# Kernel optimization log

Hardware: AMD Instinct MI355X
Metric: run time of the kernel (lower is better)

Reference implementation:

```python
import jax, jax.numpy as jnp
import numpy as np
import math

H = 8          # num_heads
DH = 16        # dim_head
DEPTH = 1
LAMBDA_INIT = 0.8 - 0.6 * math.exp(-0.3 * DEPTH)
LN_EPS = 1e-5


def setup_inputs() -> dict:
    key = jax.random.key(0)
    ks = jax.random.split(key, 12)
    dim = 256
    inner = 2 * H * DH  # 256
    b, n = 2, 2048
    s = lambda fan_in: 1.0 / math.sqrt(fan_in)
    return {
        "x": jax.random.normal(ks[0], (b, n, dim), jnp.float32),
        "Wq": jax.random.normal(ks[1], (dim, inner), jnp.float32) * s(dim),
        "Wkv": jax.random.normal(ks[2], (dim, 2 * inner), jnp.float32) * s(dim),
        "Wout": jax.random.normal(ks[3], (inner, dim), jnp.float32) * s(inner),
        "bout": jnp.zeros((dim,), jnp.float32),
        "Wg": jax.random.normal(ks[4], (dim, inner), jnp.float32) * s(dim),
        "bg": jnp.ones((inner,), jnp.float32),
        "lq1": jax.random.normal(ks[5], (DH,), jnp.float32) * 0.1,
        "lk1": jax.random.normal(ks[6], (DH,), jnp.float32) * 0.1,
        "lq2": jax.random.normal(ks[7], (DH,), jnp.float32) * 0.1,
        "lk2": jax.random.normal(ks[8], (DH,), jnp.float32) * 0.1,
        "ln_gamma": jnp.ones((2 * DH,), jnp.float32),
        "ln_beta": jnp.zeros((2 * DH,), jnp.float32),
    }


def reference(x, Wq, Wkv, Wout, bout, Wg, bg, lq1, lk1, lq2, lk2, ln_gamma, ln_beta):
    b, n, dim = x.shape
    scale = DH ** (-0.5)

    q = x @ Wq                                   # [b, n, 2*H*DH]
    kv = x @ Wkv                                 # [b, n, 4*H*DH]
    k, v = jnp.split(kv, 2, axis=-1)

    # doubled heads for q, k; normal heads with width 2*DH for v
    q = q.reshape(b, n, 2 * H, DH).transpose(0, 2, 1, 3) * scale  # [b, 2H, n, DH]
    k = k.reshape(b, n, 2 * H, DH).transpose(0, 2, 1, 3)          # [b, 2H, n, DH]
    v = v.reshape(b, n, H, 2 * DH).transpose(0, 2, 1, 3)          # [b, H, n, 2DH]

    dots = jnp.einsum('bhid,bhjd->bhij', q, k)   # [b, 2H, n, n]
    attn = jax.nn.softmax(dots, axis=-1)

    lam1 = jnp.exp(jnp.sum(lq1 * lk1))
    lam2 = jnp.exp(jnp.sum(lq2 * lk2))
    lam = lam1 - lam2 + LAMBDA_INIT

    attn = attn.reshape(b, H, 2, n, n)
    attn = attn[:, :, 0] - lam * attn[:, :, 1]   # [b, H, n, n]

    out = jnp.einsum('bhij,bhjd->bhid', attn, v)  # [b, H, n, 2DH]

    # LayerNorm over last dim (2*DH)
    mu = jnp.mean(out, axis=-1, keepdims=True)
    var = jnp.var(out, axis=-1, keepdims=True)
    out = (out - mu) * jax.lax.rsqrt(var + LN_EPS) * ln_gamma + ln_beta

    out = out * (1.0 - LAMBDA_INIT)
    out = out.transpose(0, 2, 1, 3).reshape(b, n, H * 2 * DH)  # [b, n, inner]

    gates = x @ Wg + bg
    out = out * jax.nn.sigmoid(gates)
    return out @ Wout + bout
```

## Files before the change

kernel.cpp:

```cpp
#include <hip/hip_runtime.h>
#include <hip/hip_bf16.h>

#define LAMBDA_INIT_F 0.35550906759096927f
#define ONE_MINUS_LI  0.64449093240903073f
#define QSCALE 0.36067376022224085f

typedef unsigned short u16;
typedef unsigned int   u32;
typedef short s4v  __attribute__((ext_vector_type(4)));
typedef float f16v __attribute__((ext_vector_type(16)));

__device__ __forceinline__ u16 f2bf(float f) {
    __hip_bfloat16 h = __float2bfloat16(f);
    return *reinterpret_cast<u16*>(&h);
}
__device__ __forceinline__ u32 pk2bf(float lo, float hi) {
    return (u32)f2bf(lo) | ((u32)f2bf(hi) << 16);
}
union U2S { u32 u[2]; s4v s; };
__device__ __forceinline__ s4v mks4(u32 a, u32 b) { U2S x; x.u[0]=a; x.u[1]=b; return x.s; }

__device__ __forceinline__ float fexp2(float x) {
#if __has_builtin(__builtin_amdgcn_exp2f)
    return __builtin_amdgcn_exp2f(x);
#else
    float r; asm volatile("v_exp_f32 %0, %1\n\ts_nop 1" : "=v"(r) : "v"(x)); return r;
#endif
}

#define MFMA(a,b,c) __builtin_amdgcn_mfma_f32_32x32x8bf16_1k((a),(b),(c),0,0,0)

__global__ __launch_bounds__(256) void prep_kernel(
    const float* __restrict__ Wq, const float* __restrict__ Wkv,
    const float* __restrict__ Wg, const float* __restrict__ Wout,
    const float* __restrict__ x,
    u16* __restrict__ WT, u16* __restrict__ xbf)
{
    const int bid = blockIdx.x;
    const int tid = threadIdx.x;

    if (bid >= 80) {
        const int r0 = (bid - 80) * 64;
        const float2* src = (const float2*)(x + (size_t)r0 * 256);
        u32* dst = (u32*)(xbf + (size_t)r0 * 256);
        for (int idx = tid; idx < 64 * 128; idx += 256) {
            float2 v = src[idx];
            dst[idx] = pk2bf(v.x, v.y);
        }
        return;
    }

    __shared__ u16 tile[16 * 258];
    const int n0g = bid * 16;
    const float* src; int cols; int ncol0;
    if      (n0g < 256)  { src = Wq;   cols = 256; ncol0 = n0g; }
    else if (n0g < 768)  { src = Wkv;  cols = 512; ncol0 = n0g - 256; }
    else if (n0g < 1024) { src = Wg;   cols = 256; ncol0 = n0g - 768; }
    else                 { src = Wout; cols = 256; ncol0 = n0g - 1024; }

    const float* srow = src + (size_t)tid * cols + ncol0;
#pragma unroll
    for (int j = 0; j < 8; ++j) {
        const float2 v = *(const float2*)(srow + 2*j);
        tile[(2*j + 0) * 258 + tid] = f2bf(v.x);
        tile[(2*j + 1) * 258 + tid] = f2bf(v.y);
    }
    __syncthreads();

    const u32* t32 = (const u32*)tile;
    const int nn = tid >> 4, part = tid & 15;
    u32* dst = (u32*)WT + (size_t)(n0g + nn) * 128 + part * 8;
    const u32* s2 = t32 + nn * 129 + part * 8;
#pragma unroll
    for (int j = 0; j < 8; ++j) dst[j] = s2[j];
}

__global__ __launch_bounds__(256) void proj_kernel(
    const u16* __restrict__ x, const u16* __restrict__ WT,
    const float* __restrict__ bg,
    u16* __restrict__ Qb, u16* __restrict__ Kb,
    u16* __restrict__ Vb, float* __restrict__ Gb)
{
    const int bid = blockIdx.x;
    const int nt = bid & 15, mt = bid >> 4;
    const int tid = threadIdx.x, w = tid >> 6, lane = tid & 63;
    const int l31 = lane & 31, hh = lane >> 5;
    const int m0 = mt * 128 + w * 32;
    const int n0 = nt * 64;

    const u16* xr  = x  + (size_t)(m0 + l31) * 256 + 4*hh;
    const u16* br0 = WT + (size_t)(n0 + l31) * 256 + 4*hh;
    const u16* br1 = WT + (size_t)(n0 + 32 + l31) * 256 + 4*hh;

    f16v a0, a1;
#pragma unroll
    for (int r = 0; r < 16; ++r) { a0[r] = 0.f; a1[r] = 0.f; }

#pragma unroll
    for (int ks = 0; ks < 16; ++ks) {
        s4v xa  = *(const s4v*)(xr  + ks*16);
        s4v xb  = *(const s4v*)(xr  + ks*16 + 8);
        s4v w0a = *(const s4v*)(br0 + ks*16);
        s4v w0b = *(const s4v*)(br0 + ks*16 + 8);
        s4v w1a = *(const s4v*)(br1 + ks*16);
        s4v w1b = *(const s4v*)(br1 + ks*16 + 8);
        a0 = MFMA(xa, w0a, a0); a0 = MFMA(xb, w0b, a0);
        a1 = MFMA(xa, w1a, a1); a1 = MFMA(xb, w1b, a1);
    }

    const int cat = nt >> 2;
#pragma unroll
    for (int ns = 0; ns < 2; ++ns) {
        const f16v& acc = ns ? a1 : a0;
        const int n = nt * 64 + ns * 32 + l31;
#pragma unroll
        for (int r = 0; r < 16; ++r) {
            const int il = (r & 3) + 8*(r >> 2) + 4*hh;
            const int R = m0 + il;
            const int b = R >> 11, i = R & 2047;
            const float v = acc[r];
            if (cat == 0) {
                const int h = n >> 4, d = n & 15;
                Qb[((size_t)(b*16 + h) * 2048 + i) * 16 + d] = f2bf(v * QSCALE);
            } else if (cat == 1) {
                const int nk = n - 256, h = nk >> 4, d = nk & 15;
                Kb[((size_t)(b*16 + h) * 2048 + i) * 16 + d] = f2bf(v);
            } else if (cat == 2) {
                const int nv = n - 512, hv = nv >> 5, d2 = nv & 31;
                Vb[((size_t)(b*8 + hv) * 2048 + i) * 32 + d2] = f2bf(v);
            } else {
                const int gcol = n - 768;
                const float t = v + bg[gcol];
                Gb[(size_t)R * 256 + gcol] = 1.0f / (1.0f + __expf(-t));
            }
        }
    }
}

__global__ __launch_bounds__(256) void attn_kernel(
    const u16* __restrict__ Q, const u16* __restrict__ K,
    const u16* __restrict__ V, const float* __restrict__ G,
    const float* __restrict__ lq1, const float* __restrict__ lk1,
    const float* __restrict__ lq2, const float* __restrict__ lk2,
    const float* __restrict__ gamma, const float* __restrict__ beta,
    u16* __restrict__ A)
{
    __shared__ float smemf[4480];
    u16* st  = (u16*)smemf;
    u32* stu = (u32*)smemf;

    const int bid = blockIdx.x;
    const int itile = bid & 63;
    const int combo = bid >> 6;
    const int ho = combo & 7, b = combo >> 3;
    const int i0 = itile * 32;

    const int tid = threadIdx.x, w = tid >> 6, lane = tid & 63;
    const int l31 = lane & 31, hh = lane >> 5;
    const int s = w & 1, jh = w >> 1;

    const u16* Kg = K + (size_t)(b*16 + 2*ho + s) * 2048 * 16;
    const u16* Vg = V + (size_t)(b*8 + ho) * 2048 * 32;
    const u16* Qg = Q + ((size_t)(b*16 + 2*ho + s) * 2048 + (i0 + l31)) * 16;
    const s4v qf0 = *(const s4v*)(Qg + 4*hh);
    const s4v qf1 = *(const s4v*)(Qg + 8 + 4*hh);

    const int jr = lane >> 1, half = lane & 1;
    const u32* kgp = (const u32*)Kg + (size_t)(jh*1024 + jr) * 8 + half*4;
    const u32* vgp = (const u32*)Vg + (size_t)(jh*1024 + jr) * 16 + s*8 + half*4;

    const int kw_off = w*288 + jr*9 + half*4;
    const int vw_u16 = 2304 + jh*1088;
    const int vd0 = s*16 + half*8;

    f16v oacc;
#pragma unroll
    for (int r = 0; r < 16; ++r) oacc[r] = 0.f;
    float lacc = 0.f;

    {
        u32 k0 = kgp[0], k1 = kgp[1], k2 = kgp[2], k3 = kgp[3];
        u32 v0 = vgp[0], v1 = vgp[1], v2 = vgp[2], v3 = vgp[3];
        u32* kd = stu + kw_off;
        kd[0]=k0; kd[1]=k1; kd[2]=k2; kd[3]=k3;
        u16* vd = st + vw_u16;
        vd[(vd0+0)*34 + jr] = (u16)(v0 & 0xffff); vd[(vd0+1)*34 + jr] = (u16)(v0 >> 16);
        vd[(vd0+2)*34 + jr] = (u16)(v1 & 0xffff); vd[(vd0+3)*34 + jr] = (u16)(v1 >> 16);
        vd[(vd0+4)*34 + jr] = (u16)(v2 & 0xffff); vd[(vd0+5)*34 + jr] = (u16)(v2 >> 16);
        vd[(vd0+6)*34 + jr] = (u16)(v3 & 0xffff); vd[(vd0+7)*34 + jr] = (u16)(v3 >> 16);
    }

    for (int c = 0; c < 32; ++c) {
        __syncthreads();
        const int p = c & 1, pn = 1 - p;

        u32 nk0=0,nk1=0,nk2=0,nk3=0, nv0=0,nv1=0,nv2=0,nv3=0;
        if (c + 1 < 32) {
            const u32* kp = kgp + (size_t)(c+1)*256;
            nk0=kp[0]; nk1=kp[1]; nk2=kp[2]; nk3=kp[3];
            const u32* vp = vgp + (size_t)(c+1)*512;
            nv0=vp[0]; nv1=vp[1]; nv2=vp[2]; nv3=vp[3];
        }

        const u32* kb2 = stu + p*2240 + w*288;
        const u32* vb2 = stu + p*2240 + 1152 + jh*544;

        f16v sc;
#pragma unroll
        for (int r = 0; r < 16; ++r) sc[r] = 0.f;
        {
            const int kidx = l31*9 + 2*hh;
            s4v kf0 = mks4(kb2[kidx],     kb2[kidx + 1]);
            sc = MFMA(kf0, qf0, sc);
            s4v kf1 = mks4(kb2[kidx + 4], kb2[kidx + 5]);
            sc = MFMA(kf1, qf1, sc);
        }
        float pv[16];
#pragma unroll
        for (int r = 0; r < 16; ++r) { pv[r] = fexp2(sc[r]); lacc += pv[r]; }
#pragma unroll
        for (int f = 0; f < 4; ++f) {
            u32 plo = __builtin_amdgcn_perm(__float_as_uint(pv[4*f+1]),
                                            __float_as_uint(pv[4*f+0]), 0x07060302);
            u32 phi = __builtin_amdgcn_perm(__float_as_uint(pv[4*f+3]),
                                            __float_as_uint(pv[4*f+2]), 0x07060302);
            s4v pf = mks4(plo, phi);
            const int vidx = l31*17 + 4*f + 2*hh;
            s4v vf = mks4(vb2[vidx], vb2[vidx + 1]);
            oacc = MFMA(pf, vf, oacc);
        }

        if (c + 1 < 32) {
            u32* kd = stu + pn*2240 + kw_off;
            kd[0]=nk0; kd[1]=nk1; kd[2]=nk2; kd[3]=nk3;
            u16* vd = st + pn*4480 + vw_u16;
            vd[(vd0+0)*34 + jr] = (u16)(nv0 & 0xffff); vd[(vd0+1)*34 + jr] = (u16)(nv0 >> 16);
            vd[(vd0+2)*34 + jr] = (u16)(nv1 & 0xffff); vd[(vd0+3)*34 + jr] = (u16)(nv1 >> 16);
            vd[(vd0+4)*34 + jr] = (u16)(nv2 & 0xffff); vd[(vd0+5)*34 + jr] = (u16)(nv2 >> 16);
            vd[(vd0+6)*34 + jr] = (u16)(nv3 & 0xffff); vd[(vd0+7)*34 + jr] = (u16)(nv3 >> 16);
        }
    }

    __syncthreads();
    float ltot = lacc + __shfl_xor(lacc, 32);
    float* ob = smemf + w * 1056;
#pragma unroll
    for (int r = 0; r < 16; ++r) {
        const int il = (r & 3) + 8*(r >> 2) + 4*hh;
        ob[il*33 + l31] = oacc[r];
    }
    if (lane < 32) smemf[4224 + w*32 + l31] = ltot;
    __syncthreads();

    if (tid < 32) {
        const int ii = tid;
        const float l1 = smemf[4224 + ii]      + smemf[4224 + 64 + ii];
        const float l2 = smemf[4224 + 32 + ii] + smemf[4224 + 96 + ii];

        float sA = 0.f, sB = 0.f;
#pragma unroll
        for (int d = 0; d < 16; ++d) {
            sA += lq1[d] * lk1[d];
            sB += lq2[d] * lk2[d];
        }
        const float lam = __expf(sA) - __expf(sB) + LAMBDA_INIT_F;
        const float c1 = 1.f / l1, c2 = lam / l2;

        float od[32], mu = 0.f;
#pragma unroll
        for (int d = 0; d < 32; ++d) {
            const float o1 = smemf[ii*33 + d]        + smemf[2112 + ii*33 + d];
            const float o2 = smemf[1056 + ii*33 + d] + smemf[3168 + ii*33 + d];
            od[d] = o1 * c1 - o2 * c2;
            mu += od[d];
        }
        mu *= (1.f / 32.f);
        float var = 0.f;
#pragma unroll
        for (int d = 0; d < 32; ++d) { const float t2 = od[d] - mu; var += t2 * t2; }
        var *= (1.f / 32.f);
        const float rs = rsqrtf(var + 1e-5f);

        const int R = b*2048 + i0 + ii;
        const float* Gr = G + (size_t)R * 256 + ho*32;
        u16* Ar = A + (size_t)R * 256 + ho*32;
#pragma unroll
        for (int d = 0; d < 32; ++d) {
            const float val = (od[d] - mu)*rs*gamma[d] + beta[d];
            Ar[d] = f2bf(val * ONE_MINUS_LI * Gr[d]);
        }
    }
}

__global__ __launch_bounds__(512) void out_kernel(
    const u16* __restrict__ Abf, const u16* __restrict__ WT,
    const float* __restrict__ bout, float* __restrict__ out)
{
    __shared__ float cs[4][32 * 33];

    const int bid = blockIdx.x;
    const int nt = bid & 3, mt = bid >> 2;
    const int tid = threadIdx.x, w = tid >> 6, lane = tid & 63;
    const int l31 = lane & 31, hh = lane >> 5;
    const int t = w >> 1, kh = w & 1;
    const int m0 = mt * 64 + (t & 1) * 32;
    const int n0 = nt * 64 + (t >> 1) * 32;

    const u16* ar = Abf + (size_t)(m0 + l31) * 256 + kh*128 + 4*hh;
    const u16* br = WT + (size_t)(1024 + n0 + l31) * 256 + kh*128 + 4*hh;

    f16v acc;
#pragma unroll
    for (int r = 0; r < 16; ++r) acc[r] = 0.f;

#pragma unroll
    for (int ks = 0; ks < 8; ++ks) {
        s4v aa = *(const s4v*)(ar + ks*16);
        s4v ab = *(const s4v*)(ar + ks*16 + 8);
        s4v ba = *(const s4v*)(br + ks*16);
        s4v bb = *(const s4v*)(br + ks*16 + 8);
        acc = MFMA(aa, ba, acc);
        acc = MFMA(ab, bb, acc);
    }

    if (kh == 0) {
#pragma unroll
        for (int r = 0; r < 16; ++r) {
            const int il = (r & 3) + 8*(r >> 2) + 4*hh;
            cs[t][il*33 + l31] = acc[r];
        }
    }
    __syncthreads();
    if (kh == 1) {
        const float bv = bout[n0 + l31];
#pragma unroll
        for (int r = 0; r < 16; ++r) {
            const int il = (r & 3) + 8*(r >> 2) + 4*hh;
            const int m = m0 + il;
            out[(size_t)m * 256 + n0 + l31] = acc[r] + cs[t][il*33 + l31] + bv;
        }
    }
}

extern "C" void kernel_launch(void* const* d_in, const int* in_sizes, int n_in,
                              void* d_out, int out_size, void* d_ws, size_t ws_size,
                              hipStream_t stream) {
    const float* x    = (const float*)d_in[0];
    const float* Wq   = (const float*)d_in[1];
    const float* Wkv  = (const float*)d_in[2];
    const float* Wout = (const float*)d_in[3];
    const float* bout = (const float*)d_in[4];
    const float* Wg   = (const float*)d_in[5];
    const float* bg   = (const float*)d_in[6];
    const float* lq1  = (const float*)d_in[7];
    const float* lk1  = (const float*)d_in[8];
    const float* lq2  = (const float*)d_in[9];
    const float* lk2  = (const float*)d_in[10];
    const float* lng  = (const float*)d_in[11];
    const float* lnb  = (const float*)d_in[12];

    u16*   WT  = (u16*)d_ws;
    u16*   xbf = WT + 327680;
    u16*   Qb  = xbf + 1048576;
    u16*   Kb  = Qb + 1048576;
    u16*   Vb  = Kb + 1048576;
    float* Gb  = (float*)(Vb + 1048576);
    u16*   Abf = (u16*)(Gb + 1048576);

    hipLaunchKernelGGL(prep_kernel, dim3(144), dim3(256), 0, stream,
                       Wq, Wkv, Wg, Wout, x, WT, xbf);
    hipLaunchKernelGGL(proj_kernel, dim3(512), dim3(256), 0, stream,
                       xbf, WT, bg, Qb, Kb, Vb, Gb);
    hipLaunchKernelGGL(attn_kernel, dim3(1024), dim3(256), 0, stream,
                       Qb, Kb, Vb, Gb, lq1, lk1, lq2, lk2, lng, lnb, Abf);
    hipLaunchKernelGGL(out_kernel, dim3(256), dim3(512), 0, stream,
                       Abf, WT, bout, (float*)d_out);
}
```

Baseline: 167.3 us.

## Give each wave a private K/V LDS staging region and drop block barriers

Every wave now stages its own copy of the K and V tiles in a separate double-buffered LDS region. Each lane loads a full 32-wide V row half instead of splitting it across the two sub-heads. This removes the per-iteration __syncthreads in the 32-step key loop, since a wave only reads data it wrote itself. The cost is duplicated V global loads across waves and a larger shared memory footprint (about 26 KB instead of 18 KB), which may reduce occupancy.

```diff
diff --git a/kernel.cpp b/kernel.cpp
--- a/kernel.cpp
+++ b/kernel.cpp
@@ -145,7 +145,7 @@
     const float* __restrict__ gamma, const float* __restrict__ beta,
     u16* __restrict__ A)
 {
-    __shared__ float smemf[4480];
+    __shared__ float smemf[6656];
     u16* st  = (u16*)smemf;
     u32* stu = (u32*)smemf;
 
@@ -166,12 +166,16 @@
     const s4v qf1 = *(const s4v*)(Qg + 8 + 4*hh);
 
     const int jr = lane >> 1, half = lane & 1;
+    const int vjr = lane >> 1, vhalf = lane & 1;
     const u32* kgp = (const u32*)Kg + (size_t)(jh*1024 + jr) * 8 + half*4;
-    const u32* vgp = (const u32*)Vg + (size_t)(jh*1024 + jr) * 16 + s*8 + half*4;
-
-    const int kw_off = w*288 + jr*9 + half*4;
-    const int vw_u16 = 2304 + jh*1088;
-    const int vd0 = s*16 + half*8;
+    const u32* vgp = (const u32*)Vg + (size_t)(jh*1024 + vjr) * 16 + vhalf*8;
+
+    const int wbase   = w * 1664;
+    const int kw_off  = wbase + jr*9 + half*4;
+    const int kr_off  = wbase + l31*9 + 2*hh;
+    const int vw_u16  = wbase*2 + 576 + vjr;
+    const int vr_off  = wbase + 288 + l31*17;
+    const int d0w     = vhalf * 16;
 
     f16v oacc;
 #pragma unroll
@@ -180,39 +184,44 @@
 
     {
         u32 k0 = kgp[0], k1 = kgp[1], k2 = kgp[2], k3 = kgp[3];
-        u32 v0 = vgp[0], v1 = vgp[1], v2 = vgp[2], v3 = vgp[3];
+        u32 nv[8];
+#pragma unroll
+        for (int q = 0; q < 8; ++q) nv[q] = vgp[q];
         u32* kd = stu + kw_off;
         kd[0]=k0; kd[1]=k1; kd[2]=k2; kd[3]=k3;
         u16* vd = st + vw_u16;
-        vd[(vd0+0)*34 + jr] = (u16)(v0 & 0xffff); vd[(vd0+1)*34 + jr] = (u16)(v0 >> 16);
-        vd[(vd0+2)*34 + jr] = (u16)(v1 & 0xffff); vd[(vd0+3)*34 + jr] = (u16)(v1 >> 16);
-        vd[(vd0+4)*34 + jr] = (u16)(v2 & 0xffff); vd[(vd0+5)*34 + jr] = (u16)(v2 >> 16);
-        vd[(vd0+6)*34 + jr] = (u16)(v3 & 0xffff); vd[(vd0+7)*34 + jr] = (u16)(v3 >> 16);
+#pragma unroll
+        for (int q = 0; q < 8; ++q) {
+            const int d = d0w + 2*q;
+            vd[(d+0)*34] = (u16)(nv[q] & 0xffff);
+            vd[(d+1)*34] = (u16)(nv[q] >> 16);
+        }
     }
 
     for (int c = 0; c < 32; ++c) {
-        __syncthreads();
         const int p = c & 1, pn = 1 - p;
 
-        u32 nk0=0,nk1=0,nk2=0,nk3=0, nv0=0,nv1=0,nv2=0,nv3=0;
+        u32 nk0=0,nk1=0,nk2=0,nk3=0, nv[8];
+#pragma unroll
+        for (int q = 0; q < 8; ++q) nv[q] = 0;
         if (c + 1 < 32) {
             const u32* kp = kgp + (size_t)(c+1)*256;
             nk0=kp[0]; nk1=kp[1]; nk2=kp[2]; nk3=kp[3];
             const u32* vp = vgp + (size_t)(c+1)*512;
-            nv0=vp[0]; nv1=vp[1]; nv2=vp[2]; nv3=vp[3];
-        }
-
-        const u32* kb2 = stu + p*2240 + w*288;
-        const u32* vb2 = stu + p*2240 + 1152 + jh*544;
+#pragma unroll
+            for (int q = 0; q < 8; ++q) nv[q] = vp[q];
+        }
+
+        const u32* kb2 = stu + p*832 + kr_off;
+        const u32* vb2 = stu + p*832 + vr_off;
 
         f16v sc;
 #pragma unroll
         for (int r = 0; r < 16; ++r) sc[r] = 0.f;
         {
-            const int kidx = l31*9 + 2*hh;
-            s4v kf0 = mks4(kb2[kidx],     kb2[kidx + 1]);
+            s4v kf0 = mks4(kb2[0], kb2[1]);
             sc = MFMA(kf0, qf0, sc);
-            s4v kf1 = mks4(kb2[kidx + 4], kb2[kidx + 5]);
+            s4v kf1 = mks4(kb2[4], kb2[5]);
             sc = MFMA(kf1, qf1, sc);
         }
         float pv[16];
@@ -225,19 +234,20 @@
             u32 phi = __builtin_amdgcn_perm(__float_as_uint(pv[4*f+3]),
                                             __float_as_uint(pv[4*f+2]), 0x07060302);
             s4v pf = mks4(plo, phi);
-            const int vidx = l31*17 + 4*f + 2*hh;
-            s4v vf = mks4(vb2[vidx], vb2[vidx + 1]);
+            s4v vf = mks4(vb2[4*f + 2*hh], vb2[4*f + 2*hh + 1]);
             oacc = MFMA(pf, vf, oacc);
         }
 
         if (c + 1 < 32) {
-            u32* kd = stu + pn*2240 + kw_off;
+            u32* kd = stu + pn*832 + kw_off;
             kd[0]=nk0; kd[1]=nk1; kd[2]=nk2; kd[3]=nk3;
-            u16* vd = st + pn*4480 + vw_u16;
-            vd[(vd0+0)*34 + jr] = (u16)(nv0 & 0xffff); vd[(vd0+1)*34 + jr] = (u16)(nv0 >> 16);
-            vd[(vd0+2)*34 + jr] = (u16)(nv1 & 0xffff); vd[(vd0+3)*34 + jr] = (u16)(nv1 >> 16);
-            vd[(vd0+4)*34 + jr] = (u16)(nv2 & 0xffff); vd[(vd0+5)*34 + jr] = (u16)(nv2 >> 16);
-            vd[(vd0+6)*34 + jr] = (u16)(nv3 & 0xffff); vd[(vd0+7)*34 + jr] = (u16)(nv3 >> 16);
+            u16* vd = st + pn*1664 + vw_u16;
+#pragma unroll
+            for (int q = 0; q < 8; ++q) {
+                const int d = d0w + 2*q;
+                vd[(d+0)*34] = (u16)(nv[q] & 0xffff);
+                vd[(d+1)*34] = (u16)(nv[q] >> 16);
+            }
         }
     }
 
```

Result: no change. 166.1 us (-0.7%).

## Split attention work across query tiles instead of key halves to share K/V tiles

Applied to the files above, without the earlier changes.

The attention kernel now gives each block 64 query rows, split across warp pairs, instead of 32 query rows with the key range split between warp pairs. Every warp now walks all 64 key chunks, and the staged K/V tiles in shared memory are shared by both query sub-tiles, which halves global K/V traffic per query row and halves the grid. The row-sum accumulator is also split into two independent chains to shorten dependency latency. In exchange each warp runs twice as many serial loop iterations with more barriers, grid occupancy drops to 512 blocks, and the final combine stage uses 64 threads.

```diff
diff --git a/kernel.cpp b/kernel.cpp
--- a/kernel.cpp
+++ b/kernel.cpp
@@ -150,74 +150,76 @@
     u32* stu = (u32*)smemf;
 
     const int bid = blockIdx.x;
-    const int itile = bid & 63;
-    const int combo = bid >> 6;
+    const int itile = bid & 31;
+    const int combo = bid >> 5;
     const int ho = combo & 7, b = combo >> 3;
-    const int i0 = itile * 32;
+    const int i0 = itile * 64;
 
     const int tid = threadIdx.x, w = tid >> 6, lane = tid & 63;
     const int l31 = lane & 31, hh = lane >> 5;
-    const int s = w & 1, jh = w >> 1;
-
-    const u16* Kg = K + (size_t)(b*16 + 2*ho + s) * 2048 * 16;
+    const int s = w & 1, it = w >> 1;
+    const int i0w = i0 + it * 32;
+
     const u16* Vg = V + (size_t)(b*8 + ho) * 2048 * 32;
-    const u16* Qg = Q + ((size_t)(b*16 + 2*ho + s) * 2048 + (i0 + l31)) * 16;
+    const u16* Qg = Q + ((size_t)(b*16 + 2*ho + s) * 2048 + (i0w + l31)) * 16;
     const s4v qf0 = *(const s4v*)(Qg + 4*hh);
     const s4v qf1 = *(const s4v*)(Qg + 8 + 4*hh);
 
-    const int jr = lane >> 1, half = lane & 1;
-    const u32* kgp = (const u32*)Kg + (size_t)(jh*1024 + jr) * 8 + half*4;
-    const u32* vgp = (const u32*)Vg + (size_t)(jh*1024 + jr) * 16 + s*8 + half*4;
-
-    const int kw_off = w*288 + jr*9 + half*4;
-    const int vw_u16 = 2304 + jh*1088;
-    const int vd0 = s*16 + half*8;
+    const int ksub = tid >> 7, krow = (tid >> 2) & 31, kseg = tid & 3;
+    const u32* kgp = (const u32*)(K + (size_t)(b*16 + 2*ho + ksub) * 2048 * 16)
+                     + (size_t)krow * 8 + kseg * 2;
+    const int vj = tid >> 3, vd4 = (tid & 7) * 4;
+    const u32* vgp = (const u32*)Vg + (size_t)vj * 16 + (tid & 7) * 2;
+
+    const int kw_off = ksub*288 + krow*9 + kseg*2;
+    const int kr_off = s*288 + l31*9 + 2*hh;
+    const int vr_off = 576 + l31*17;
+    const int vw_u16 = 1152 + vd4*34 + vj;
 
     f16v oacc;
 #pragma unroll
     for (int r = 0; r < 16; ++r) oacc[r] = 0.f;
-    float lacc = 0.f;
+    float la0 = 0.f, la1 = 0.f;
 
     {
-        u32 k0 = kgp[0], k1 = kgp[1], k2 = kgp[2], k3 = kgp[3];
-        u32 v0 = vgp[0], v1 = vgp[1], v2 = vgp[2], v3 = vgp[3];
+        u32 k0 = kgp[0], k1 = kgp[1];
+        u32 v0 = vgp[0], v1 = vgp[1];
         u32* kd = stu + kw_off;
-        kd[0]=k0; kd[1]=k1; kd[2]=k2; kd[3]=k3;
+        kd[0] = k0; kd[1] = k1;
         u16* vd = st + vw_u16;
-        vd[(vd0+0)*34 + jr] = (u16)(v0 & 0xffff); vd[(vd0+1)*34 + jr] = (u16)(v0 >> 16);
-        vd[(vd0+2)*34 + jr] = (u16)(v1 & 0xffff); vd[(vd0+3)*34 + jr] = (u16)(v1 >> 16);
-        vd[(vd0+4)*34 + jr] = (u16)(v2 & 0xffff); vd[(vd0+5)*34 + jr] = (u16)(v2 >> 16);
-        vd[(vd0+6)*34 + jr] = (u16)(v3 & 0xffff); vd[(vd0+7)*34 + jr] = (u16)(v3 >> 16);
-    }
-
-    for (int c = 0; c < 32; ++c) {
+        vd[0]    = (u16)(v0 & 0xffff); vd[34]    = (u16)(v0 >> 16);
+        vd[68]   = (u16)(v1 & 0xffff); vd[102]   = (u16)(v1 >> 16);
+    }
+
+    for (int c = 0; c < 64; ++c) {
         __syncthreads();
         const int p = c & 1, pn = 1 - p;
-
-        u32 nk0=0,nk1=0,nk2=0,nk3=0, nv0=0,nv1=0,nv2=0,nv3=0;
-        if (c + 1 < 32) {
-            const u32* kp = kgp + (size_t)(c+1)*256;
-            nk0=kp[0]; nk1=kp[1]; nk2=kp[2]; nk3=kp[3];
-            const u32* vp = vgp + (size_t)(c+1)*512;
-            nv0=vp[0]; nv1=vp[1]; nv2=vp[2]; nv3=vp[3];
-        }
-
-        const u32* kb2 = stu + p*2240 + w*288;
-        const u32* vb2 = stu + p*2240 + 1152 + jh*544;
+        const int cc = (c + 1) & 63;
+
+        const u32* kp = kgp + (size_t)cc * 256;
+        u32 nk0 = kp[0], nk1 = kp[1];
+        const u32* vp = vgp + (size_t)cc * 512;
+        u32 nv0 = vp[0], nv1 = vp[1];
+
+        const u32* kb2 = stu + p*1120 + kr_off;
+        const u32* vb2 = stu + p*1120 + vr_off;
 
         f16v sc;
 #pragma unroll
         for (int r = 0; r < 16; ++r) sc[r] = 0.f;
         {
-            const int kidx = l31*9 + 2*hh;
-            s4v kf0 = mks4(kb2[kidx],     kb2[kidx + 1]);
+            s4v kf0 = mks4(kb2[0], kb2[1]);
             sc = MFMA(kf0, qf0, sc);
-            s4v kf1 = mks4(kb2[kidx + 4], kb2[kidx + 5]);
+            s4v kf1 = mks4(kb2[4], kb2[5]);
             sc = MFMA(kf1, qf1, sc);
         }
         float pv[16];
 #pragma unroll
-        for (int r = 0; r < 16; ++r) { pv[r] = fexp2(sc[r]); lacc += pv[r]; }
+        for (int r = 0; r < 16; ++r) pv[r] = fexp2(sc[r]);
+        la0 += pv[0];  la0 += pv[1];  la0 += pv[2];  la0 += pv[3];
+        la1 += pv[4];  la1 += pv[5];  la1 += pv[6];  la1 += pv[7];
+        la0 += pv[8];  la0 += pv[9];  la0 += pv[10]; la0 += pv[11];
+        la1 += pv[12]; la1 += pv[13]; la1 += pv[14]; la1 += pv[15];
 #pragma unroll
         for (int f = 0; f < 4; ++f) {
             u32 plo = __builtin_amdgcn_perm(__float_as_uint(pv[4*f+1]),
@@ -225,21 +227,19 @@
             u32 phi = __builtin_amdgcn_perm(__float_as_uint(pv[4*f+3]),
                                             __float_as_uint(pv[4*f+2]), 0x07060302);
             s4v pf = mks4(plo, phi);
-            const int vidx = l31*17 + 4*f + 2*hh;
-            s4v vf = mks4(vb2[vidx], vb2[vidx + 1]);
+            s4v vf = mks4(vb2[4*f + 2*hh], vb2[4*f + 2*hh + 1]);
             oacc = MFMA(pf, vf, oacc);
         }
 
-        if (c + 1 < 32) {
-            u32* kd = stu + pn*2240 + kw_off;
-            kd[0]=nk0; kd[1]=nk1; kd[2]=nk2; kd[3]=nk3;
-            u16* vd = st + pn*4480 + vw_u16;
-            vd[(vd0+0)*34 + jr] = (u16)(nv0 & 0xffff); vd[(vd0+1)*34 + jr] = (u16)(nv0 >> 16);
-            vd[(vd0+2)*34 + jr] = (u16)(nv1 & 0xffff); vd[(vd0+3)*34 + jr] = (u16)(nv1 >> 16);
-            vd[(vd0+4)*34 + jr] = (u16)(nv2 & 0xffff); vd[(vd0+5)*34 + jr] = (u16)(nv2 >> 16);
-            vd[(vd0+6)*34 + jr] = (u16)(nv3 & 0xffff); vd[(vd0+7)*34 + jr] = (u16)(nv3 >> 16);
-        }
-    }
+        {
+            u32* kd = stu + pn*1120 + kw_off;
+            kd[0] = nk0; kd[1] = nk1;
+            u16* vd = st + pn*2240 + vw_u16;
+            vd[0]  = (u16)(nv0 & 0xffff); vd[34]  = (u16)(nv0 >> 16);
+            vd[68] = (u16)(nv1 & 0xffff); vd[102] = (u16)(nv1 >> 16);
+        }
+    }
+    const float lacc = la0 + la1;
 
     __syncthreads();
     float ltot = lacc + __shfl_xor(lacc, 32);
@@ -252,10 +252,12 @@
     if (lane < 32) smemf[4224 + w*32 + l31] = ltot;
     __syncthreads();
 
-    if (tid < 32) {
-        const int ii = tid;
-        const float l1 = smemf[4224 + ii]      + smemf[4224 + 64 + ii];
-        const float l2 = smemf[4224 + 32 + ii] + smemf[4224 + 96 + ii];
+    if (tid < 64) {
+        const int it2 = tid >> 5, ii = tid & 31;
+        const float l1 = smemf[4224 + (2*it2 + 0)*32 + ii];
+        const float l2 = smemf[4224 + (2*it2 + 1)*32 + ii];
+        const float* o1 = smemf + (2*it2 + 0)*1056 + ii*33;
+        const float* o2 = smemf + (2*it2 + 1)*1056 + ii*33;
 
         float sA = 0.f, sB = 0.f;
 #pragma unroll
@@ -269,9 +271,7 @@
         float od[32], mu = 0.f;
 #pragma unroll
         for (int d = 0; d < 32; ++d) {
-            const float o1 = smemf[ii*33 + d]        + smemf[2112 + ii*33 + d];
-            const float o2 = smemf[1056 + ii*33 + d] + smemf[3168 + ii*33 + d];
-            od[d] = o1 * c1 - o2 * c2;
+            od[d] = o1[d] * c1 - o2[d] * c2;
             mu += od[d];
         }
         mu *= (1.f / 32.f);
@@ -281,7 +281,7 @@
         var *= (1.f / 32.f);
         const float rs = rsqrtf(var + 1e-5f);
 
-        const int R = b*2048 + i0 + ii;
+        const int R = b*2048 + i0 + it2*32 + ii;
         const float* Gr = G + (size_t)R * 256 + ho*32;
         u16* Ar = A + (size_t)R * 256 + ho*32;
 #pragma unroll
@@ -371,7 +371,7 @@
                        Wq, Wkv, Wg, Wout, x, WT, xbf);
     hipLaunchKernelGGL(proj_kernel, dim3(512), dim3(256), 0, stream,
                        xbf, WT, bg, Qb, Kb, Vb, Gb);
-    hipLaunchKernelGGL(attn_kernel, dim3(1024), dim3(256), 0, stream,
+    hipLaunchKernelGGL(attn_kernel, dim3(512), dim3(256), 0, stream,
                        Qb, Kb, Vb, Gb, lq1, lk1, lq2, lk2, lng, lnb, Abf);
     hipLaunchKernelGGL(out_kernel, dim3(256), dim3(512), 0, stream,
                        Abf, WT, bout, (float*)d_out);
```

After: 175.8 us. +5.1%, slower.

## Split attention key range across four wave pairs with 512-thread blocks

Applied to the files above, without the earlier changes.

Doubles the attention block to 512 threads (8 waves). The key/value range is now split into four quarters instead of two, so each wave pair runs 16 iterations rather than 32. The shared staging buffers double in size, and the epilogue reduces partial outputs and row sums over four quarters. The row-sum accumulation is also split into two independent chains to shorten the dependency. The aim is more waves in flight per query tile, at the cost of more shared memory, a larger final reduction, and one redundant wrap-around prefetch on the last iteration.

```diff
diff --git a/kernel.cpp b/kernel.cpp
--- a/kernel.cpp
+++ b/kernel.cpp
@@ -137,7 +137,7 @@
     }
 }
 
-__global__ __launch_bounds__(256) void attn_kernel(
+__global__ __launch_bounds__(512, 8) void attn_kernel(
     const u16* __restrict__ Q, const u16* __restrict__ K,
     const u16* __restrict__ V, const float* __restrict__ G,
     const float* __restrict__ lq1, const float* __restrict__ lk1,
@@ -145,7 +145,7 @@
     const float* __restrict__ gamma, const float* __restrict__ beta,
     u16* __restrict__ A)
 {
-    __shared__ float smemf[4480];
+    __shared__ float smemf[8960];
     u16* st  = (u16*)smemf;
     u32* stu = (u32*)smemf;
 
@@ -157,26 +157,31 @@
 
     const int tid = threadIdx.x, w = tid >> 6, lane = tid & 63;
     const int l31 = lane & 31, hh = lane >> 5;
-    const int s = w & 1, jh = w >> 1;
-
-    const u16* Kg = K + (size_t)(b*16 + 2*ho + s) * 2048 * 16;
+    const int s = w & 1, jq = w >> 1;
+
     const u16* Vg = V + (size_t)(b*8 + ho) * 2048 * 32;
     const u16* Qg = Q + ((size_t)(b*16 + 2*ho + s) * 2048 + (i0 + l31)) * 16;
     const s4v qf0 = *(const s4v*)(Qg + 4*hh);
     const s4v qf1 = *(const s4v*)(Qg + 8 + 4*hh);
 
-    const int jr = lane >> 1, half = lane & 1;
-    const u32* kgp = (const u32*)Kg + (size_t)(jh*1024 + jr) * 8 + half*4;
-    const u32* vgp = (const u32*)Vg + (size_t)(jh*1024 + jr) * 16 + s*8 + half*4;
-
-    const int kw_off = w*288 + jr*9 + half*4;
-    const int vw_u16 = 2304 + jh*1088;
-    const int vd0 = s*16 + half*8;
+    const int qp = tid >> 7;
+    const int pid = tid & 127;
+    const int ksub = pid >> 6, krow = (pid >> 1) & 31, kseg = pid & 1;
+    const u32* kgp = (const u32*)(K + (size_t)(b*16 + 2*ho + ksub) * 2048 * 16)
+                     + (size_t)qp * 4096 + krow * 8 + kseg * 4;
+    const int vj = pid >> 2, vseg = pid & 3;
+    const u32* vgp = (const u32*)Vg + (size_t)qp * 8192 + vj * 16 + vseg * 4;
+
+    const int kw_off = qp*1120 + ksub*288 + krow*9 + kseg*4;
+    const int vw_u16 = qp*2240 + 1152 + vj;
+    const int vd0 = vseg * 8;
+    const int kr_off = jq*1120 + s*288 + l31*9 + 2*hh;
+    const int vr_off = jq*1120 + 576 + l31*17;
 
     f16v oacc;
 #pragma unroll
     for (int r = 0; r < 16; ++r) oacc[r] = 0.f;
-    float lacc = 0.f;
+    float la0 = 0.f, la1 = 0.f;
 
     {
         u32 k0 = kgp[0], k1 = kgp[1], k2 = kgp[2], k3 = kgp[3];
@@ -184,40 +189,41 @@
         u32* kd = stu + kw_off;
         kd[0]=k0; kd[1]=k1; kd[2]=k2; kd[3]=k3;
         u16* vd = st + vw_u16;
-        vd[(vd0+0)*34 + jr] = (u16)(v0 & 0xffff); vd[(vd0+1)*34 + jr] = (u16)(v0 >> 16);
-        vd[(vd0+2)*34 + jr] = (u16)(v1 & 0xffff); vd[(vd0+3)*34 + jr] = (u16)(v1 >> 16);
-        vd[(vd0+4)*34 + jr] = (u16)(v2 & 0xffff); vd[(vd0+5)*34 + jr] = (u16)(v2 >> 16);
-        vd[(vd0+6)*34 + jr] = (u16)(v3 & 0xffff); vd[(vd0+7)*34 + jr] = (u16)(v3 >> 16);
-    }
-
-    for (int c = 0; c < 32; ++c) {
+        vd[(vd0+0)*34] = (u16)(v0 & 0xffff); vd[(vd0+1)*34] = (u16)(v0 >> 16);
+        vd[(vd0+2)*34] = (u16)(v1 & 0xffff); vd[(vd0+3)*34] = (u16)(v1 >> 16);
+        vd[(vd0+4)*34] = (u16)(v2 & 0xffff); vd[(vd0+5)*34] = (u16)(v2 >> 16);
+        vd[(vd0+6)*34] = (u16)(v3 & 0xffff); vd[(vd0+7)*34] = (u16)(v3 >> 16);
+    }
+
+    for (int t = 0; t < 16; ++t) {
         __syncthreads();
-        const int p = c & 1, pn = 1 - p;
-
-        u32 nk0=0,nk1=0,nk2=0,nk3=0, nv0=0,nv1=0,nv2=0,nv3=0;
-        if (c + 1 < 32) {
-            const u32* kp = kgp + (size_t)(c+1)*256;
-            nk0=kp[0]; nk1=kp[1]; nk2=kp[2]; nk3=kp[3];
-            const u32* vp = vgp + (size_t)(c+1)*512;
-            nv0=vp[0]; nv1=vp[1]; nv2=vp[2]; nv3=vp[3];
-        }
-
-        const u32* kb2 = stu + p*2240 + w*288;
-        const u32* vb2 = stu + p*2240 + 1152 + jh*544;
+        const int p = t & 1, pn = 1 - p;
+        const int tt = (t + 1) & 15;
+
+        const u32* kp = kgp + (size_t)tt * 256;
+        u32 nk0=kp[0], nk1=kp[1], nk2=kp[2], nk3=kp[3];
+        const u32* vp = vgp + (size_t)tt * 512;
+        u32 nv0=vp[0], nv1=vp[1], nv2=vp[2], nv3=vp[3];
+
+        const u32* kb2 = stu + p*4480 + kr_off;
+        const u32* vb2 = stu + p*4480 + vr_off;
 
         f16v sc;
 #pragma unroll
         for (int r = 0; r < 16; ++r) sc[r] = 0.f;
         {
-            const int kidx = l31*9 + 2*hh;
-            s4v kf0 = mks4(kb2[kidx],     kb2[kidx + 1]);
+            s4v kf0 = mks4(kb2[0], kb2[1]);
             sc = MFMA(kf0, qf0, sc);
-            s4v kf1 = mks4(kb2[kidx + 4], kb2[kidx + 5]);
+            s4v kf1 = mks4(kb2[4], kb2[5]);
             sc = MFMA(kf1, qf1, sc);
         }
         float pv[16];
 #pragma unroll
-        for (int r = 0; r < 16; ++r) { pv[r] = fexp2(sc[r]); lacc += pv[r]; }
+        for (int r = 0; r < 16; ++r) pv[r] = fexp2(sc[r]);
+        la0 += pv[0];  la0 += pv[1];  la0 += pv[2];  la0 += pv[3];
+        la1 += pv[4];  la1 += pv[5];  la1 += pv[6];  la1 += pv[7];
+        la0 += pv[8];  la0 += pv[9];  la0 += pv[10]; la0 += pv[11];
+        la1 += pv[12]; la1 += pv[13]; la1 += pv[14]; la1 += pv[15];
 #pragma unroll
         for (int f = 0; f < 4; ++f) {
             u32 plo = __builtin_amdgcn_perm(__float_as_uint(pv[4*f+1]),
@@ -225,21 +231,21 @@
             u32 phi = __builtin_amdgcn_perm(__float_as_uint(pv[4*f+3]),
                                             __float_as_uint(pv[4*f+2]), 0x07060302);
             s4v pf = mks4(plo, phi);
-            const int vidx = l31*17 + 4*f + 2*hh;
-            s4v vf = mks4(vb2[vidx], vb2[vidx + 1]);
+            s4v vf = mks4(vb2[4*f + 2*hh], vb2[4*f + 2*hh + 1]);
             oacc = MFMA(pf, vf, oacc);
         }
 
-        if (c + 1 < 32) {
-            u32* kd = stu + pn*2240 + kw_off;
+        {
+            u32* kd = stu + pn*4480 + kw_off;
             kd[0]=nk0; kd[1]=nk1; kd[2]=nk2; kd[3]=nk3;
-            u16* vd = st + pn*4480 + vw_u16;
-            vd[(vd0+0)*34 + jr] = (u16)(nv0 & 0xffff); vd[(vd0+1)*34 + jr] = (u16)(nv0 >> 16);
-            vd[(vd0+2)*34 + jr] = (u16)(nv1 & 0xffff); vd[(vd0+3)*34 + jr] = (u16)(nv1 >> 16);
-            vd[(vd0+4)*34 + jr] = (u16)(nv2 & 0xffff); vd[(vd0+5)*34 + jr] = (u16)(nv2 >> 16);
-            vd[(vd0+6)*34 + jr] = (u16)(nv3 & 0xffff); vd[(vd0+7)*34 + jr] = (u16)(nv3 >> 16);
-        }
-    }
+            u16* vd = st + pn*8960 + vw_u16;
+            vd[(vd0+0)*34] = (u16)(nv0 & 0xffff); vd[(vd0+1)*34] = (u16)(nv0 >> 16);
+            vd[(vd0+2)*34] = (u16)(nv1 & 0xffff); vd[(vd0+3)*34] = (u16)(nv1 >> 16);
+            vd[(vd0+4)*34] = (u16)(nv2 & 0xffff); vd[(vd0+5)*34] = (u16)(nv2 >> 16);
+            vd[(vd0+6)*34] = (u16)(nv3 & 0xffff); vd[(vd0+7)*34] = (u16)(nv3 >> 16);
+        }
+    }
+    const float lacc = la0 + la1;
 
     __syncthreads();
     float ltot = lacc + __shfl_xor(lacc, 32);
@@ -249,13 +255,17 @@
         const int il = (r & 3) + 8*(r >> 2) + 4*hh;
         ob[il*33 + l31] = oacc[r];
     }
-    if (lane < 32) smemf[4224 + w*32 + l31] = ltot;
+    if (lane < 32) smemf[8448 + w*32 + l31] = ltot;
     __syncthreads();
 
     if (tid < 32) {
         const int ii = tid;
-        const float l1 = smemf[4224 + ii]      + smemf[4224 + 64 + ii];
-        const float l2 = smemf[4224 + 32 + ii] + smemf[4224 + 96 + ii];
+        float l1 = 0.f, l2 = 0.f;
+#pragma unroll
+        for (int q = 0; q < 4; ++q) {
+            l1 += smemf[8448 + (2*q + 0)*32 + ii];
+            l2 += smemf[8448 + (2*q + 1)*32 + ii];
+        }
 
         float sA = 0.f, sB = 0.f;
 #pragma unroll
@@ -269,8 +279,12 @@
         float od[32], mu = 0.f;
 #pragma unroll
         for (int d = 0; d < 32; ++d) {
-            const float o1 = smemf[ii*33 + d]        + smemf[2112 + ii*33 + d];
-            const float o2 = smemf[1056 + ii*33 + d] + smemf[3168 + ii*33 + d];
+            float o1 = 0.f, o2 = 0.f;
+#pragma unroll
+            for (int q = 0; q < 4; ++q) {
+                o1 += smemf[(2*q + 0)*1056 + ii*33 + d];
+                o2 += smemf[(2*q + 1)*1056 + ii*33 + d];
+            }
             od[d] = o1 * c1 - o2 * c2;
             mu += od[d];
         }
@@ -371,7 +385,7 @@
                        Wq, Wkv, Wg, Wout, x, WT, xbf);
     hipLaunchKernelGGL(proj_kernel, dim3(512), dim3(256), 0, stream,
                        xbf, WT, bg, Qb, Kb, Vb, Gb);
-    hipLaunchKernelGGL(attn_kernel, dim3(1024), dim3(256), 0, stream,
+    hipLaunchKernelGGL(attn_kernel, dim3(1024), dim3(512), 0, stream,
                        Qb, Kb, Vb, Gb, lq1, lk1, lq2, lk2, lng, lnb, Abf);
     hipLaunchKernelGGL(out_kernel, dim3(256), dim3(512), 0, stream,
                        Abf, WT, bout, (float*)d_out);
```

Result: faster. 158.5 us (-5.3%).
